# Kernel tuning notes

Measured on AMD Instinct MI355X. Metric: run time of the kernel, lower is better.

Reference implementation:

```python
import jax, jax.numpy as jnp
import numpy as np

NC1, NC2 = 97, 300   # EPIC-Kitchens verb / noun class counts
T_FRAMES = 24000     # frames in one long video
N_ACTIONS = 3806     # (verb, noun) action pairs in mapping.txt
HID = 512            # cfg.hid_dim


def setup_inputs() -> dict:
    key = jax.random.key(0)
    k1, k2, k3 = jax.random.split(key, 3)
    H = HID + NC1 + NC2  # 909: hidden features with class logits appended
    frame_feature = jax.random.normal(k1, (T_FRAMES, 1, H), dtype=jnp.float32)
    vids = jax.random.randint(k2, (N_ACTIONS,), 0, NC1, dtype=jnp.int32)
    nids = jax.random.randint(k3, (N_ACTIONS,), 0, NC2, dtype=jnp.int32)
    return {"frame_feature": frame_feature, "vids": vids, "nids": nids}


def _combine_verb_noun(clogit, vids, nids):
    # combine_verb_noun_to_action with apply_log=True:
    # log_softmax verbs and nouns separately, gather per action id, add.
    vlog = jax.nn.log_softmax(clogit[..., :NC1], axis=-1)
    nlog = jax.nn.log_softmax(clogit[..., NC1:], axis=-1)
    return vlog[..., vids] + nlog[..., nids]


def reference(frame_feature, vids, nids):
    T = frame_feature.shape[0]
    # --- verb/noun softmax-gather-multiply combine (frame level) ---
    clogit = frame_feature[..., -NC1 - NC2:]                 # [T,1,NC1+NC2]
    frame_logp = _combine_verb_noun(clogit, vids, nids)      # [T,1,A]

    # --- parse_label: segment ids from per-frame argmax prediction ---
    pred = jnp.argmax(frame_logp[:, 0], axis=-1)             # [T]
    change = jnp.concatenate(
        [jnp.zeros((1,), jnp.int32), (pred[1:] != pred[:-1]).astype(jnp.int32)]
    )
    seg_id = jax.lax.stop_gradient(jnp.cumsum(change))       # [T], in [0, nseg)

    # --- TemporalDownsampleUpsample.feature_frame2seg: mean-pool per segment ---
    feat = frame_feature[:, 0]                               # [T,H]
    seg_sum = jax.ops.segment_sum(feat, seg_id, num_segments=T)
    cnt = jax.ops.segment_sum(jnp.ones((T, 1), feat.dtype), seg_id, num_segments=T)
    seg_feat = seg_sum / jnp.maximum(cnt, 1.0)               # [T,H] (padded segments)

    # segment-level verb/noun combine
    seg_logp = _combine_verb_noun(seg_feat[:, -NC1 - NC2:], vids, nids)  # [T,A]

    # --- feature_seg2frame: broadcast segment values back to frames ---
    s2f = seg_logp[seg_id]                                   # [T,A]
    return frame_logp + s2f[:, None, :]                      # [T,1,A]
```

## Files before the change

### kernel.cpp

```cpp
#include <hip/hip_runtime.h>
#include <math.h>

#define T_FRAMES 24000
#define NC1 97
#define NC2 300
#define NCC 397
#define NA 3806
#define NA_PAD 3808
#define NSORT 4096
#define H_DIM 909
#define COFF 512
#define TAB 400


__device__ __forceinline__ float waveMax(float v) {
#pragma unroll
    for (int off = 32; off > 0; off >>= 1) v = fmaxf(v, __shfl_xor(v, off));
    return v;
}

__device__ __forceinline__ float waveSum(float v) {
#pragma unroll
    for (int off = 32; off > 0; off >>= 1) v += __shfl_xor(v, off);
    return v;
}

__device__ __forceinline__ unsigned flip32(float f) {
    unsigned u = __float_as_uint(f);
    return (u & 0x80000000u) ? ~u : (u | 0x80000000u);
}


__global__ __launch_bounds__(256) void k_prep(const int* __restrict__ vids,
                                              const int* __restrict__ nids,
                                              int* __restrict__ pk,
                                              unsigned* __restrict__ skey) {
    __shared__ unsigned cnt[NC2];
    __shared__ unsigned ofs[NC2];
    const int tid = threadIdx.x;

    for (int i = tid; i < NC2; i += 256) cnt[i] = 0u;
    __syncthreads();

    for (int a = tid; a < NA; a += 256) {
        int v = vids[a], n = nids[a];
        pk[a] = v | (n << 16);
        atomicAdd(&cnt[n], 1u);
    }
    __syncthreads();

    if (tid < 64) {
        unsigned run = 0;
        for (int c = 0; c < 5; c++) {
            int i = c * 64 + tid;
            unsigned x = (i < NC2) ? cnt[i] : 0u;
            unsigned inc = x;
#pragma unroll
            for (int d = 1; d < 64; d <<= 1) {
                unsigned y = __shfl_up(inc, d);
                if (tid >= d) inc += y;
            }
            if (i < NC2) ofs[i] = run + inc - x;
            run += __shfl(inc, 63);
        }
    }
    __syncthreads();

    for (int a = tid; a < NA; a += 256) {
        unsigned v = (unsigned)vids[a], n = (unsigned)nids[a];
        unsigned p = atomicAdd(&ofs[n], 1u);
        skey[p] = (n << 19) | (v << 12) | (unsigned)a;
    }
    for (int i = NA + tid; i < NSORT; i += 256) skey[i] = 0xFFFFFFFFu;
}


__global__ __launch_bounds__(256) void k_frame(const float* __restrict__ ff,
                                               const unsigned* __restrict__ skey,
                                               float2* __restrict__ fstats,
                                               int* __restrict__ pred) {
    const int tid = threadIdx.x;
    const int wid = tid >> 6, lane = tid & 63;
    const int t = blockIdx.x * 4 + wid;

    __shared__ float sh[4][TAB];
    float* S = sh[wid];

    const float* row = ff + (size_t)t * H_DIM + COFF;

    float xv[7];
    float vmax = -INFINITY, nmax = -INFINITY;
#pragma unroll
    for (int j = 0; j < 7; j++) {
        const int idx = lane + j * 64;
        float x = -INFINITY;
        if (idx < NCC) { x = row[idx]; S[idx] = x; }
        xv[j] = x;
        if (idx < NC1) vmax = fmaxf(vmax, x);
        else           nmax = fmaxf(nmax, x);
    }
    vmax = waveMax(vmax);
    nmax = waveMax(nmax);

    float vs = 0.f, ns = 0.f;
#pragma unroll
    for (int j = 0; j < 7; j++) {
        const int idx = lane + j * 64;
        if (idx < NC1)      vs += __expf(xv[j] - vmax);
        else if (idx < NCC) ns += __expf(xv[j] - nmax);
    }
    vs = waveSum(vs);
    ns = waveSum(ns);
    const float c1 = vmax + __logf(vs);
    const float c2 = nmax + __logf(ns);

    const uint4* sk4 = (const uint4*)skey;
    unsigned long long best = 0ull;
    for (int g = lane; g < NSORT / 4; g += 64) {
        const uint4 kq = sk4[g];
        const unsigned ks[4] = {kq.x, kq.y, kq.z, kq.w};
#pragma unroll
        for (int j = 0; j < 4; j++) {
            const unsigned kk = ks[j];
            if (kk != 0xFFFFFFFFu) {
                const float val = S[(kk >> 12) & 0x7Fu] + S[NC1 + (kk >> 19)];
                const unsigned long long rk =
                    ((unsigned long long)flip32(val) << 32) | ((~kk) & 0xFFFu);
                best = (rk > best) ? rk : best;
            }
        }
    }
#pragma unroll
    for (int off = 32; off > 0; off >>= 1) {
        unsigned long long o = __shfl_xor(best, off);
        best = (o > best) ? o : best;
    }

    if (lane == 0) {
        pred[t] = (int)((~(unsigned)best) & 0xFFFu);
        fstats[t] = make_float2(c1, c2);
    }
}


__global__ __launch_bounds__(1024) void k_scan(const int* __restrict__ pred,
                                               int* __restrict__ seg_start,
                                               int* __restrict__ Scount) {
    const int tid = threadIdx.x;
    __shared__ unsigned short flg[T_FRAMES];
    __shared__ int wsum[16];

    for (int t = tid; t < T_FRAMES; t += 1024)
        flg[t] = (unsigned short)((t > 0) ? (pred[t] != pred[t - 1]) : 0);
    __syncthreads();

    const int CH = (T_FRAMES + 1023) / 1024;
    const int base = tid * CH;
    int cnt = 0;
    for (int k = 0; k < CH; k++) {
        int t = base + k;
        if (t < T_FRAMES) cnt += flg[t];
    }
    const int lane = tid & 63, wid = tid >> 6;
    int inc = cnt;
#pragma unroll
    for (int d = 1; d < 64; d <<= 1) {
        int n = __shfl_up(inc, d);
        if (lane >= d) inc += n;
    }
    if (lane == 63) wsum[wid] = inc;
    __syncthreads();
    if (tid == 0) {
        int acc = 0;
        for (int i = 0; i < 16; i++) { int x = wsum[i]; wsum[i] = acc; acc += x; }
    }
    __syncthreads();
    int sid = wsum[wid] + inc - cnt;

    for (int k = 0; k < CH; k++) {
        int t = base + k;
        if (t >= T_FRAMES) break;
        if (t == 0) seg_start[0] = 0;
        else if (flg[t]) { sid++; seg_start[sid] = t; }
        if (t == T_FRAMES - 1) *Scount = sid + 1;
    }
}


__global__ __launch_bounds__(256) void k_segout(const float* __restrict__ ff,
                                                const int* __restrict__ pk,
                                                const float2* __restrict__ fstats,
                                                const int* __restrict__ seg_start,
                                                const int* __restrict__ Scount,
                                                float* __restrict__ out) {
    const int tid = threadIdx.x;
    const int wid = tid >> 6, lane = tid & 63;
    const int s = blockIdx.x * 4 + wid;
    const int S = *Scount;
    if (s >= S) return;

    const int start = seg_start[s];
    int end = (s + 1 < S) ? seg_start[s + 1] : T_FRAMES;
    if (end > T_FRAMES) end = T_FRAMES;
    const int len = end - start;

    float acc[7] = {0.f, 0.f, 0.f, 0.f, 0.f, 0.f, 0.f};
    const float* basep = ff + (size_t)start * H_DIM + COFF;
    for (int k = 0; k < len; k++) {
        const float* p = basep + (size_t)k * H_DIM;
#pragma unroll
        for (int j = 0; j < 7; j++) {
            const int idx = lane + j * 64;
            if (idx < NCC) acc[j] += p[idx];
        }
    }
    const float inv = 1.f / (float)len;

    float lp[7];
    float vmax = -INFINITY, nmax = -INFINITY;
#pragma unroll
    for (int j = 0; j < 7; j++) {
        const int idx = lane + j * 64;
        float x = (idx < NCC) ? acc[j] * inv : -INFINITY;
        lp[j] = x;
        if (idx < NC1) vmax = fmaxf(vmax, x);
        else           nmax = fmaxf(nmax, x);
    }
    vmax = waveMax(vmax);
    nmax = waveMax(nmax);
    float vs = 0.f, ns = 0.f;
#pragma unroll
    for (int j = 0; j < 7; j++) {
        const int idx = lane + j * 64;
        if (idx < NC1)      vs += __expf(lp[j] - vmax);
        else if (idx < NCC) ns += __expf(lp[j] - nmax);
    }
    vs = waveSum(vs);
    ns = waveSum(ns);
    const float cv = vmax + __logf(vs);
    const float cn = nmax + __logf(ns);
#pragma unroll
    for (int j = 0; j < 7; j++) {
        const int idx = lane + j * 64;
        lp[j] -= (idx < NC1) ? cv : cn;
    }

    __shared__ float sh[4][TAB];
    float* Stab = sh[wid];
    const int2* pk2 = (const int2*)pk;

    for (int t = start; t < end; t++) {
        const float2 c = fstats[t];
        const float* row = ff + (size_t)t * H_DIM + COFF;
#pragma unroll
        for (int j = 0; j < 7; j++) {
            const int idx = lane + j * 64;
            if (idx < NCC)
                Stab[idx] = row[idx] + lp[j] - ((idx < NC1) ? c.x : c.y);
        }
        float* orow = out + (size_t)t * NA;
        for (int g = lane; g < NA / 2; g += 64) {
            const int2 p2 = pk2[g];
            float2 o;
            o.x = Stab[p2.x & 0xffff] + Stab[NC1 + (p2.x >> 16)];
            o.y = Stab[p2.y & 0xffff] + Stab[NC1 + (p2.y >> 16)];
            *(float2*)(orow + 2 * g) = o;
        }
    }
}


extern "C" void kernel_launch(void* const* d_in, const int* in_sizes, int n_in,
                              void* d_out, int out_size, void* d_ws, size_t ws_size,
                              hipStream_t stream) {
    const float* ff = (const float*)d_in[0];
    const int* vids = (const int*)d_in[1];
    const int* nids = (const int*)d_in[2];
    float* out = (float*)d_out;

    char* ws = (char*)d_ws;
    size_t off = 0;
    float2* fstats = (float2*)(ws + off);  off += (size_t)T_FRAMES * 8;
    int* pred = (int*)(ws + off);          off += (size_t)T_FRAMES * 4;
    int* seg_start = (int*)(ws + off);     off += (size_t)T_FRAMES * 4;
    int* Scount = (int*)(ws + off);        off += 16;
    int* pk = (int*)(ws + off);            off += (size_t)NA_PAD * 4;
    unsigned* skey = (unsigned*)(ws + off); off += (size_t)NSORT * 4;

    k_prep<<<1, 256, 0, stream>>>(vids, nids, pk, skey);
    k_frame<<<T_FRAMES / 4, 256, 0, stream>>>(ff, skey, fstats, pred);
    k_scan<<<1, 1024, 0, stream>>>(pred, seg_start, Scount);
    k_segout<<<T_FRAMES / 4, 256, 0, stream>>>(ff, pk, fstats, seg_start, Scount, out);
}
```

Baseline: 521.3 us.

## Fuse all stages into one cooperative persistent kernel with grid syncs

Replaces the four launches (prep, frame argmax, single-block scan, segment output) with one cooperative kernel. Each block builds the sorted action key table in shared memory, then works through frames persistently, runs a distributed block-count scan between grid-wide syncs, and finishes with the segment pooling and output writes. This removes launch gaps and the serial 1-block scan, at the cost of redundant per-block table construction, grid sync overhead, and a grid limited to at most 4 blocks per CU times 256. The original multi-kernel path is kept as a fallback if the cooperative launch fails.

```diff
diff --git a/kernel.cpp b/kernel.cpp
--- a/kernel.cpp
+++ b/kernel.cpp
@@ -1,5 +1,8 @@
 #include <hip/hip_runtime.h>
+#include <hip/hip_cooperative_groups.h>
 #include <math.h>
+
+namespace cg = cooperative_groups;
 
 #define T_FRAMES 24000
 #define NC1 97
@@ -11,6 +14,7 @@
 #define H_DIM 909
 #define COFF 512
 #define TAB 400
+#define SENT_NID 300u
 
 
 __device__ __forceinline__ float waveMax(float v) {
@@ -31,24 +35,39 @@
 }
 
 
-__global__ __launch_bounds__(256) void k_prep(const int* __restrict__ vids,
-                                              const int* __restrict__ nids,
-                                              int* __restrict__ pk,
-                                              unsigned* __restrict__ skey) {
+__global__ __launch_bounds__(256, 4) void k_all(
+    const float* __restrict__ ff,
+    const int* __restrict__ vids,
+    const int* __restrict__ nids,
+    int* __restrict__ pk,
+    float2* __restrict__ fstats,
+    int* __restrict__ pred,
+    int* __restrict__ seg_start,
+    int* __restrict__ blockCnt,
+    int* __restrict__ blockOfs,
+    int* __restrict__ Scnt,
+    float* __restrict__ out)
+{
+    const int tid = threadIdx.x;
+    const int wid = tid >> 6, lane = tid & 63;
+    const int b = blockIdx.x;
+    const int NBLK = gridDim.x;
+    const int NW = NBLK * 4;
+    const int gw = b * 4 + wid;
+
+    __shared__ float sh[4][TAB];
+    __shared__ unsigned skey[NA_PAD];
     __shared__ unsigned cnt[NC2];
     __shared__ unsigned ofs[NC2];
-    const int tid = threadIdx.x;
 
     for (int i = tid; i < NC2; i += 256) cnt[i] = 0u;
     __syncthreads();
-
-    for (int a = tid; a < NA; a += 256) {
-        int v = vids[a], n = nids[a];
-        pk[a] = v | (n << 16);
-        atomicAdd(&cnt[n], 1u);
-    }
-    __syncthreads();
-
+    for (int a = tid; a < NA; a += 256) atomicAdd(&cnt[nids[a]], 1u);
+    if (b == 0) {
+        for (int a = tid; a < NA_PAD; a += 256)
+            pk[a] = (a < NA) ? (vids[a] | (nids[a] << 16)) : 0;
+    }
+    __syncthreads();
     if (tid < 64) {
         unsigned run = 0;
         for (int c = 0; c < 5; c++) {
@@ -65,18 +84,227 @@
         }
     }
     __syncthreads();
-
     for (int a = tid; a < NA; a += 256) {
         unsigned v = (unsigned)vids[a], n = (unsigned)nids[a];
         unsigned p = atomicAdd(&ofs[n], 1u);
         skey[p] = (n << 19) | (v << 12) | (unsigned)a;
     }
-    for (int i = NA + tid; i < NSORT; i += 256) skey[i] = 0xFFFFFFFFu;
-}
-
+    for (int i = NA + tid; i < NA_PAD; i += 256) skey[i] = (SENT_NID << 19);
+    __syncthreads();
+
+    float* S = sh[wid];
+    const uint4* sk4 = (const uint4*)skey;
+
+    for (int t = gw; t < T_FRAMES; t += NW) {
+        const float* row = ff + (size_t)t * H_DIM + COFF;
+        float xv[7];
+        float vmax = -INFINITY, nmax = -INFINITY;
+#pragma unroll
+        for (int j = 0; j < 7; j++) {
+            const int idx = lane + j * 64;
+            float x = -INFINITY;
+            if (idx < NCC)      { x = row[idx]; S[idx] = x; }
+            else if (idx < TAB) { S[idx] = -INFINITY; }
+            xv[j] = x;
+            if (idx < NC1) vmax = fmaxf(vmax, x);
+            else           nmax = fmaxf(nmax, x);
+        }
+        vmax = waveMax(vmax);
+        nmax = waveMax(nmax);
+
+        float vs = 0.f, ns = 0.f;
+#pragma unroll
+        for (int j = 0; j < 7; j++) {
+            const int idx = lane + j * 64;
+            if (idx < NC1)      vs += __expf(xv[j] - vmax);
+            else if (idx < NCC) ns += __expf(xv[j] - nmax);
+        }
+        vs = waveSum(vs);
+        ns = waveSum(ns);
+        const float c1 = vmax + __logf(vs);
+        const float c2 = nmax + __logf(ns);
+
+        unsigned long long best = 0ull;
+        for (int g = lane; g < NA_PAD / 4; g += 64) {
+            const uint4 kq = sk4[g];
+            const unsigned ks[4] = {kq.x, kq.y, kq.z, kq.w};
+#pragma unroll
+            for (int jj = 0; jj < 4; jj++) {
+                const unsigned kk = ks[jj];
+                const float val = S[(kk >> 12) & 0x7Fu] + S[NC1 + (kk >> 19)];
+                const unsigned long long rk =
+                    ((unsigned long long)flip32(val) << 32) | ((~kk) & 0xFFFu);
+                best = (rk > best) ? rk : best;
+            }
+        }
+#pragma unroll
+        for (int off = 32; off > 0; off >>= 1) {
+            unsigned long long o = __shfl_xor(best, off);
+            best = (o > best) ? o : best;
+        }
+        if (lane == 0) {
+            pred[t] = (int)((~(unsigned)best) & 0xFFFu);
+            fstats[t] = make_float2(c1, c2);
+        }
+    }
+
+    cg::this_grid().sync();
+
+    const int CH = (T_FRAMES + NBLK - 1) / NBLK;
+    if (wid == 0) {
+        int t = b * CH + lane;
+        int flag = (lane < CH && t > 0 && t < T_FRAMES) ? (pred[t] != pred[t - 1]) : 0;
+        unsigned long long m = __ballot(flag);
+        if (lane == 0) blockCnt[b] = __popcll(m);
+    }
+    cg::this_grid().sync();
+
+    if (b == 0 && wid == 0) {
+        int run = 0;
+        const int NCHK = (NBLK + 63) / 64;
+        for (int c = 0; c < NCHK; c++) {
+            int i = c * 64 + lane;
+            int x = (i < NBLK) ? blockCnt[i] : 0;
+            int inc = x;
+#pragma unroll
+            for (int d = 1; d < 64; d <<= 1) {
+                int y = __shfl_up(inc, d);
+                if (lane >= d) inc += y;
+            }
+            if (i < NBLK) blockOfs[i] = run + inc - x;
+            run += __shfl(inc, 63);
+        }
+        if (lane == 0) *Scnt = run + 1;
+    }
+    cg::this_grid().sync();
+
+    if (wid == 0) {
+        const int base = blockOfs[b];
+        int t = b * CH + lane;
+        int flag = (lane < CH && t > 0 && t < T_FRAMES) ? (pred[t] != pred[t - 1]) : 0;
+        unsigned long long m = __ballot(flag);
+        if (flag) {
+            int lp_ = __popcll(m & ((1ull << lane) - 1ull));
+            seg_start[base + lp_ + 1] = t;
+        }
+        if (b == 0 && lane == 0) seg_start[0] = 0;
+    }
+    cg::this_grid().sync();
+
+    const int S_ = *Scnt;
+    const int2* pk2 = (const int2*)pk;
+
+    for (int s = gw; s < S_; s += NW) {
+        const int start = seg_start[s];
+        int end = (s + 1 < S_) ? seg_start[s + 1] : T_FRAMES;
+        if (end > T_FRAMES) end = T_FRAMES;
+        const int len = end - start;
+
+        float acc[7] = {0.f, 0.f, 0.f, 0.f, 0.f, 0.f, 0.f};
+        const float* basep = ff + (size_t)start * H_DIM + COFF;
+        for (int k = 0; k < len; k++) {
+            const float* p = basep + (size_t)k * H_DIM;
+#pragma unroll
+            for (int j = 0; j < 7; j++) {
+                const int idx = lane + j * 64;
+                if (idx < NCC) acc[j] += p[idx];
+            }
+        }
+        const float inv = 1.f / (float)len;
+
+        float lp[7];
+        float vmax = -INFINITY, nmax = -INFINITY;
+#pragma unroll
+        for (int j = 0; j < 7; j++) {
+            const int idx = lane + j * 64;
+            float x = (idx < NCC) ? acc[j] * inv : -INFINITY;
+            lp[j] = x;
+            if (idx < NC1) vmax = fmaxf(vmax, x);
+            else           nmax = fmaxf(nmax, x);
+        }
+        vmax = waveMax(vmax);
+        nmax = waveMax(nmax);
+        float vs = 0.f, ns = 0.f;
+#pragma unroll
+        for (int j = 0; j < 7; j++) {
+            const int idx = lane + j * 64;
+            if (idx < NC1)      vs += __expf(lp[j] - vmax);
+            else if (idx < NCC) ns += __expf(lp[j] - nmax);
+        }
+        vs = waveSum(vs);
+        ns = waveSum(ns);
+        const float cv = vmax + __logf(vs);
+        const float cn = nmax + __logf(ns);
+#pragma unroll
+        for (int j = 0; j < 7; j++) {
+            const int idx = lane + j * 64;
+            lp[j] -= (idx < NC1) ? cv : cn;
+        }
+
+        for (int t = start; t < end; t++) {
+            const float2 c = fstats[t];
+            const float* row = ff + (size_t)t * H_DIM + COFF;
+#pragma unroll
+            for (int j = 0; j < 7; j++) {
+                const int idx = lane + j * 64;
+                if (idx < NCC)
+                    S[idx] = row[idx] + lp[j] - ((idx < NC1) ? c.x : c.y);
+            }
+            float* orow = out + (size_t)t * NA;
+            for (int g = lane; g < NA / 2; g += 64) {
+                const int2 p2 = pk2[g];
+                float2 o;
+                o.x = S[p2.x & 0xffff] + S[NC1 + (p2.x >> 16)];
+                o.y = S[p2.y & 0xffff] + S[NC1 + (p2.y >> 16)];
+                *(float2*)(orow + 2 * g) = o;
+            }
+        }
+    }
+}
+
+
+__global__ __launch_bounds__(256) void k_prep(const int* __restrict__ vids,
+                                              const int* __restrict__ nids,
+                                              int* __restrict__ pk,
+                                              unsigned* __restrict__ skeyg) {
+    __shared__ unsigned cnt[NC2];
+    __shared__ unsigned ofs[NC2];
+    const int tid = threadIdx.x;
+
+    for (int i = tid; i < NC2; i += 256) cnt[i] = 0u;
+    __syncthreads();
+    for (int a = tid; a < NA; a += 256) {
+        int v = vids[a], n = nids[a];
+        pk[a] = v | (n << 16);
+        atomicAdd(&cnt[n], 1u);
+    }
+    __syncthreads();
+    if (tid < 64) {
+        unsigned run = 0;
+        for (int c = 0; c < 5; c++) {
+            int i = c * 64 + tid;
+            unsigned x = (i < NC2) ? cnt[i] : 0u;
+            unsigned inc = x;
+#pragma unroll
+            for (int d = 1; d < 64; d <<= 1) {
+                unsigned y = __shfl_up(inc, d);
+                if (tid >= d) inc += y;
+            }
+            if (i < NC2) ofs[i] = run + inc - x;
+            run += __shfl(inc, 63);
+        }
+    }
+    __syncthreads();
+    for (int a = tid; a < NA; a += 256) {
+        unsigned v = (unsigned)vids[a], n = (unsigned)nids[a];
+        unsigned p = atomicAdd(&ofs[n], 1u);
+        skeyg[p] = (n << 19) | (v << 12) | (unsigned)a;
+    }
+    for (int i = NA + tid; i < NSORT; i += 256) skeyg[i] = 0xFFFFFFFFu;
+}
 
 __global__ __launch_bounds__(256) void k_frame(const float* __restrict__ ff,
-                                               const unsigned* __restrict__ skey,
+                                               const unsigned* __restrict__ skeyg,
                                                float2* __restrict__ fstats,
                                                int* __restrict__ pred) {
     const int tid = threadIdx.x;
@@ -85,7 +313,6 @@
 
     __shared__ float sh[4][TAB];
     float* S = sh[wid];
-
     const float* row = ff + (size_t)t * H_DIM + COFF;
 
     float xv[7];
@@ -101,7 +328,6 @@
     }
     vmax = waveMax(vmax);
     nmax = waveMax(nmax);
-
     float vs = 0.f, ns = 0.f;
 #pragma unroll
     for (int j = 0; j < 7; j++) {
@@ -114,7 +340,7 @@
     const float c1 = vmax + __logf(vs);
     const float c2 = nmax + __logf(ns);
 
-    const uint4* sk4 = (const uint4*)skey;
+    const uint4* sk4 = (const uint4*)skeyg;
     unsigned long long best = 0ull;
     for (int g = lane; g < NSORT / 4; g += 64) {
         const uint4 kq = sk4[g];
@@ -135,13 +361,11 @@
         unsigned long long o = __shfl_xor(best, off);
         best = (o > best) ? o : best;
     }
-
     if (lane == 0) {
         pred[t] = (int)((~(unsigned)best) & 0xFFFu);
         fstats[t] = make_float2(c1, c2);
     }
 }
-
 
 __global__ __launch_bounds__(1024) void k_scan(const int* __restrict__ pred,
                                                int* __restrict__ seg_start,
@@ -185,7 +409,6 @@
         if (t == T_FRAMES - 1) *Scount = sid + 1;
     }
 }
-
 
 __global__ __launch_bounds__(256) void k_segout(const float* __restrict__ ff,
                                                 const int* __restrict__ pk,
@@ -280,15 +503,37 @@
 
     char* ws = (char*)d_ws;
     size_t off = 0;
-    float2* fstats = (float2*)(ws + off);  off += (size_t)T_FRAMES * 8;
-    int* pred = (int*)(ws + off);          off += (size_t)T_FRAMES * 4;
-    int* seg_start = (int*)(ws + off);     off += (size_t)T_FRAMES * 4;
-    int* Scount = (int*)(ws + off);        off += 16;
-    int* pk = (int*)(ws + off);            off += (size_t)NA_PAD * 4;
-    unsigned* skey = (unsigned*)(ws + off); off += (size_t)NSORT * 4;
-
-    k_prep<<<1, 256, 0, stream>>>(vids, nids, pk, skey);
-    k_frame<<<T_FRAMES / 4, 256, 0, stream>>>(ff, skey, fstats, pred);
-    k_scan<<<1, 1024, 0, stream>>>(pred, seg_start, Scount);
-    k_segout<<<T_FRAMES / 4, 256, 0, stream>>>(ff, pk, fstats, seg_start, Scount, out);
-}
+    float2* fstats = (float2*)(ws + off);   off += (size_t)T_FRAMES * 8;
+    int* pred = (int*)(ws + off);           off += (size_t)T_FRAMES * 4;
+    int* seg_start = (int*)(ws + off);      off += (size_t)T_FRAMES * 4;
+    int* Scnt = (int*)(ws + off);           off += 16;
+    int* pk = (int*)(ws + off);             off += (size_t)NA_PAD * 4;
+    int* blockCnt = (int*)(ws + off);       off += 1024 * 4;
+    int* blockOfs = (int*)(ws + off);       off += 1024 * 4;
+    unsigned* skeyg = (unsigned*)(ws + off); off += (size_t)NSORT * 4;
+
+    static int maxb = 0;
+    if (maxb == 0) {
+        int q = 0;
+        if (hipOccupancyMaxActiveBlocksPerMultiprocessor(&q, (const void*)k_all,
+                                                         256, 0) != hipSuccess || q < 2)
+            q = 2;
+        if (q > 4) q = 4;
+        maxb = q;
+    }
+    const int grid = maxb * 256;
+
+    void* args[] = { (void*)&ff, (void*)&vids, (void*)&nids, (void*)&pk,
+                     (void*)&fstats, (void*)&pred, (void*)&seg_start,
+                     (void*)&blockCnt, (void*)&blockOfs, (void*)&Scnt,
+                     (void*)&out };
+
+    hipError_t err = hipLaunchCooperativeKernel((const void*)k_all, dim3(grid),
+                                                dim3(256), args, 0, stream);
+    if (err != hipSuccess) {
+        k_prep<<<1, 256, 0, stream>>>(vids, nids, pk, skeyg);
+        k_frame<<<T_FRAMES / 4, 256, 0, stream>>>(ff, skeyg, fstats, pred);
+        k_scan<<<1, 1024, 0, stream>>>(pred, seg_start, Scnt);
+        k_segout<<<T_FRAMES / 4, 256, 0, stream>>>(ff, pk, fstats, seg_start, Scnt, out);
+    }
+}
```

Result: slower. 837.4 us (+60.6%).
